# Performance work log

Measured on AMD Instinct MI355X. Metric: run time of the kernel, lower is better.

The kernel has to match this reference:

```python
import jax, jax.numpy as jnp
import numpy as np

HEAD_DIM = 64  # config['head_dim']
# dropout_prob=0.1 is a no-op in eval mode; reference computes deterministic attention.

def setup_inputs() -> dict:
    key = jax.random.key(0)
    kq, kk, kv = jax.random.split(key, 3)
    shape = (2, 12, 2048, HEAD_DIM)  # [batch, heads, seq, head_dim]
    Q = jax.random.normal(kq, shape, dtype=jnp.float32)
    K = jax.random.normal(kk, shape, dtype=jnp.float32)
    V = jax.random.normal(kv, shape, dtype=jnp.float32)
    return {"Q": Q, "K": K, "V": V}

def reference(Q, K, V):
    # dot = Q @ K^T / sqrt(head_dim); attn = softmax(dot); X = attn @ V
    scale = 1.0 / np.float32(np.sqrt(HEAD_DIM))
    dot = jnp.einsum('bhqd,bhkd->bhqk', Q, K) * scale  # [B,H,S,S]
    attn = jax.nn.softmax(dot, axis=-1)
    X = jnp.einsum('bhqk,bhkd->bhqd', attn, V)
    return X
```

## Files before the change

kernel.cpp:

```cpp
#include <hip/hip_runtime.h>
#include <hip/hip_bf16.h>

typedef __attribute__((ext_vector_type(8))) short bf16x8;
typedef __attribute__((ext_vector_type(4))) float f32x4;
typedef __attribute__((ext_vector_type(4))) unsigned short u16x4;
typedef __attribute__((ext_vector_type(2))) unsigned int u32x2;
typedef __attribute__((ext_vector_type(4))) unsigned int u32x4;
typedef __attribute__((ext_vector_type(4))) _Float16 f16x4;
typedef __attribute__((ext_vector_type(2))) __fp16 h16x2;
typedef __attribute__((ext_vector_type(4))) __fp16 h16x4;

#define SEQ 2048
#define HD 64
#define BH 24

__device__ __forceinline__ unsigned bfpack(float a, float b) {
  union { float f; unsigned u; } ua, ub; ua.f = a; ub.f = b;
  return __builtin_amdgcn_perm(ub.u + 0x8000u, ua.u + 0x8000u, 0x07060302u);
}
__device__ __forceinline__ unsigned short f2bf(float f) {
  union { float f; unsigned u; } v; v.f = f;
  unsigned r = v.u + 0x7fffu + ((v.u >> 16) & 1u);
  return (unsigned short)(r >> 16);
}

__global__ __launch_bounds__(256) void prep_kv(const float* __restrict__ K,
                                               const float* __restrict__ V,
                                               unsigned* __restrict__ Kb,
                                               _Float16* __restrict__ Vt) {
  __shared__ _Float16 t[64 * 68];
  const int bid = blockIdx.x;
  const int sb = bid >> 3;
  const int bh = (bid & 7) * 3 + (sb >> 5);
  const int k0 = (sb & 31) * 64;
  const int tid = threadIdx.x;

  const float4* ks = (const float4*)(K + ((size_t)bh * SEQ + k0) * HD);
  unsigned* kd = Kb + ((size_t)bh * SEQ + k0) * (HD / 2);
#pragma unroll
  for (int i = 0; i < 4; ++i) {
    int f = tid + i * 256;
    float4 v = ks[f];
    u32x2 o;
    o.x = bfpack(v.x, v.y);
    o.y = bfpack(v.z, v.w);
    *(u32x2*)&kd[f * 2] = o;
  }

  const float4* vs = (const float4*)(V + ((size_t)bh * SEQ + k0) * HD);
#pragma unroll
  for (int i = 0; i < 4; ++i) {
    int f = tid + i * 256;
    int k = f >> 4, cg = f & 15;
    float4 v = vs[k * 16 + cg];
    int dg = cg * 4;
    t[(dg + 0) * 68 + k] = (_Float16)v.x;
    t[(dg + 1) * 68 + k] = (_Float16)v.y;
    t[(dg + 2) * 68 + k] = (_Float16)v.z;
    t[(dg + 3) * 68 + k] = (_Float16)v.w;
  }
  __syncthreads();
  int d = tid >> 2, kg = (tid & 3) * 16;
  _Float16* g = Vt + ((size_t)(bh * 64 + d)) * SEQ + k0 + kg;
#pragma unroll
  for (int r = 0; r < 4; ++r) {
    f16x4 x = *(f16x4*)&t[d * 68 + kg + r * 4];
    *(f16x4*)&g[r * 4] = x;
  }
}

__global__ __launch_bounds__(256, 3) void attn_main(const float* __restrict__ Q,
                                                    const unsigned short* __restrict__ Kb,
                                                    const _Float16* __restrict__ Vt,
                                                    float* __restrict__ O) {
  __shared__ unsigned short kv[3][8192];

  const int tid  = threadIdx.x;
  const int lane = tid & 63;
  const int w    = tid >> 6;
  const int quad = lane >> 4;
  const int n    = lane & 15;

  const int bid = blockIdx.x;
  const int sb = bid >> 3;
  const int bh = (bid & 7) * 3 + (sb >> 5);
  const int q0 = (sb & 31) * 64;

  const float qscale = 0.125f * 1.44269504088896f;

  bf16x8 qf[4][2];
#pragma unroll
  for (int u = 0; u < 4; ++u) {
    const float* qb = Q + ((size_t)bh * SEQ + q0 + u * 16 + n) * HD;
#pragma unroll
    for (int h = 0; h < 2; ++h) {
      float4 a = *(const float4*)(qb + h * 32 + quad * 8);
      float4 b = *(const float4*)(qb + h * 32 + quad * 8 + 4);
      u32x4 pk;
      pk.x = bfpack(a.x * qscale, a.y * qscale);
      pk.y = bfpack(a.z * qscale, a.w * qscale);
      pk.z = bfpack(b.x * qscale, b.y * qscale);
      pk.w = bfpack(b.z * qscale, b.w * qscale);
      qf[u][h] = __builtin_bit_cast(bf16x8, pk);
    }
  }

  const unsigned short* Kbase = Kb + (size_t)bh * SEQ * HD;
  const unsigned short* Vbase = (const unsigned short*)(Vt + (size_t)bh * HD * SEQ);
  const unsigned short* ksrc[2];
  const unsigned short* vsrc[2];
  int soff[2];
#pragma unroll
  for (int i = 0; i < 2; ++i) {
    int s = i * 256 + tid;
    int r = s >> 3, p = s & 7, G = p ^ (r & 7);
    ksrc[i] = Kbase + r * HD + G * 8;
    vsrc[i] = Vbase + (size_t)r * SEQ + G * 8;
    soff[i] = s * 8;
  }

#define DMA_TO(buf_, it_)                                                                 \
  {                                                                                       \
    unsigned short* db_ = &kv[buf_][0];                                                   \
    _Pragma("unroll")                                                                     \
    for (int i_ = 0; i_ < 2; ++i_) {                                                      \
      __builtin_amdgcn_global_load_lds(                                                   \
          (const __attribute__((address_space(1))) void*)(ksrc[i_] + (size_t)(it_) * 4096), \
          (__attribute__((address_space(3))) void*)(db_ + soff[i_]), 16, 0, 0);           \
      __builtin_amdgcn_global_load_lds(                                                   \
          (const __attribute__((address_space(1))) void*)(vsrc[i_] + (size_t)(it_) * 64), \
          (__attribute__((address_space(3))) void*)(db_ + 4096 + soff[i_]), 16, 0, 0);    \
    }                                                                                     \
    asm volatile("" ::: "memory");                                                        \
  }

  f32x4 o[4][4];
#pragma unroll
  for (int dt = 0; dt < 4; ++dt)
#pragma unroll
    for (int u = 0; u < 4; ++u) o[dt][u] = (f32x4){0.f, 0.f, 0.f, 0.f};
  float lsum[4] = {0.f, 0.f, 0.f, 0.f};

  int ro[2];
#pragma unroll
  for (int h = 0; h < 2; ++h) ro[h] = n * 64 + (((h * 4 + quad) ^ (n & 7)) * 8);
  int vo[4];
#pragma unroll
  for (int dt = 0; dt < 4; ++dt)
    vo[dt] = dt * 1024 + n * 64 + (((w * 2 + (quad >> 1)) ^ (n & 7)) * 8) + (quad & 1) * 4;

#define COMPUTE(buf_)                                                                     \
  {                                                                                       \
    const unsigned short* kb = &kv[buf_][0];                                              \
    const unsigned short* vb = kb + 4096;                                                 \
    f32x4 s[4] = {{0,0,0,0},{0,0,0,0},{0,0,0,0},{0,0,0,0}};                               \
    _Pragma("unroll")                                                                     \
    for (int h = 0; h < 2; ++h) {                                                         \
      bf16x8 a = *(const bf16x8*)&kb[w * 1024 + ro[h]];                                   \
      _Pragma("unroll")                                                                   \
      for (int u = 0; u < 4; ++u)                                                         \
        s[u] = __builtin_amdgcn_mfma_f32_16x16x32_bf16(a, qf[u][h], s[u], 0, 0, 0);       \
    }                                                                                     \
    f16x4 pf[4];                                                                          \
    _Pragma("unroll")                                                                     \
    for (int u = 0; u < 4; ++u) {                                                         \
      float e0 = __builtin_amdgcn_exp2f(s[u][0]);                                         \
      float e1 = __builtin_amdgcn_exp2f(s[u][1]);                                         \
      float e2 = __builtin_amdgcn_exp2f(s[u][2]);                                         \
      float e3 = __builtin_amdgcn_exp2f(s[u][3]);                                         \
      lsum[u] += (e0 + e1) + (e2 + e3);                                                   \
      h16x2 a_ = __builtin_amdgcn_cvt_pkrtz(e0, e1);                                      \
      h16x2 b_ = __builtin_amdgcn_cvt_pkrtz(e2, e3);                                      \
      h16x4 ab_ = __builtin_shufflevector(a_, b_, 0, 1, 2, 3);                            \
      pf[u] = __builtin_bit_cast(f16x4, ab_);                                             \
    }                                                                                     \
    _Pragma("unroll")                                                                     \
    for (int dt = 0; dt < 4; ++dt) {                                                      \
      f16x4 vf = *(const f16x4*)((const _Float16*)vb + vo[dt]);                           \
      _Pragma("unroll")                                                                   \
      for (int u = 0; u < 4; ++u)                                                         \
        o[dt][u] = __builtin_amdgcn_mfma_f32_16x16x16f16(vf, pf[u], o[dt][u], 0, 0, 0);   \
    }                                                                                     \
  }

  DMA_TO(0, 0);
  DMA_TO(1, 1);

  int bc = 0;
  int bd = 2;
  for (int it = 0; it < 31; ++it) {
    asm volatile("s_waitcnt vmcnt(4)\n\ts_barrier" ::: "memory");
    if (it < 30) DMA_TO(bd, it + 2);
    COMPUTE(bc);
    bc = (bc == 2) ? 0 : bc + 1;
    bd = (bd == 2) ? 0 : bd + 1;
  }
  asm volatile("s_waitcnt vmcnt(0)\n\ts_barrier" ::: "memory");
  COMPUTE(bc);

#undef DMA_TO
#undef COMPUTE

#pragma unroll
  for (int u = 0; u < 4; ++u) {
    lsum[u] += __shfl_xor(lsum[u], 16);
    lsum[u] += __shfl_xor(lsum[u], 32);
  }

  float* red = (float*)&kv[0][0];
  float* lred = red + 2 * 4096;

  __syncthreads();
  if (w & 1) {
    int s = w >> 1;
#pragma unroll
    for (int dt = 0; dt < 4; ++dt)
#pragma unroll
      for (int u = 0; u < 4; ++u)
        *(f32x4*)&red[s * 4096 + (dt * 4 + u) * 256 + lane * 4] = o[dt][u];
#pragma unroll
    for (int u = 0; u < 4; ++u) lred[s * 256 + u * 64 + lane] = lsum[u];
  }
  __syncthreads();
  if (!(w & 1)) {
    int s = w >> 1;
#pragma unroll
    for (int dt = 0; dt < 4; ++dt)
#pragma unroll
      for (int u = 0; u < 4; ++u)
        o[dt][u] += *(f32x4*)&red[s * 4096 + (dt * 4 + u) * 256 + lane * 4];
#pragma unroll
    for (int u = 0; u < 4; ++u) lsum[u] += lred[s * 256 + u * 64 + lane];
  }
  __syncthreads();
  if (w == 2) {
#pragma unroll
    for (int dt = 0; dt < 4; ++dt)
#pragma unroll
      for (int u = 0; u < 4; ++u)
        *(f32x4*)&red[4096 + (dt * 4 + u) * 256 + lane * 4] = o[dt][u];
#pragma unroll
    for (int u = 0; u < 4; ++u) lred[256 + u * 64 + lane] = lsum[u];
  }
  __syncthreads();
  if (w == 0) {
#pragma unroll
    for (int dt = 0; dt < 4; ++dt)
#pragma unroll
      for (int u = 0; u < 4; ++u)
        o[dt][u] += *(f32x4*)&red[4096 + (dt * 4 + u) * 256 + lane * 4];
#pragma unroll
    for (int u = 0; u < 4; ++u) {
      float inv = 1.0f / (lsum[u] + lred[256 + u * 64 + lane]);
      float* og = O + ((size_t)bh * SEQ + q0 + u * 16 + n) * HD + quad * 4;
#pragma unroll
      for (int dt = 0; dt < 4; ++dt) {
        f32x4 r = o[dt][u];
        r.x *= inv; r.y *= inv; r.z *= inv; r.w *= inv;
        *(f32x4*)(og + dt * 16) = r;
      }
    }
  }
}

#define F_QT 128
#define F_KT 64
#define F_LD 72

__global__ __launch_bounds__(512) void attn_fwd(const float* __restrict__ Q,
                                                const float* __restrict__ K,
                                                const float* __restrict__ V,
                                                float* __restrict__ O) {
  __shared__ unsigned short sm[(F_QT + F_KT + HD + 8 * 16) * F_LD];
  unsigned short* Qs = sm;
  unsigned short* Ks = Qs + F_QT * F_LD;
  unsigned short* Vt = Ks + F_KT * F_LD;
  unsigned short* Ps = Vt + HD * F_LD;

  const int tid = threadIdx.x, lane = tid & 63, wv = tid >> 6;
  const int quad = lane >> 4, n = lane & 15;
  const int bh = blockIdx.y, q0 = blockIdx.x * F_QT;
  const float* Qg = Q + ((size_t)bh * SEQ + q0) * HD;
  const float* Kg = K + (size_t)bh * SEQ * HD;
  const float* Vg = V + (size_t)bh * SEQ * HD;
  float* Og = O + ((size_t)bh * SEQ + q0) * HD;
  const float qscale = 0.125f * 1.44269504088896f;

#pragma unroll
  for (int i = 0; i < 4; ++i) {
    int f = tid + i * 512;
    int row = f >> 4, cg = f & 15;
    float4 qv = ((const float4*)Qg)[row * 16 + cg];
    u16x4 h;
    h.x = f2bf(qv.x * qscale); h.y = f2bf(qv.y * qscale);
    h.z = f2bf(qv.z * qscale); h.w = f2bf(qv.w * qscale);
    *(u16x4*)&Qs[row * F_LD + cg * 4] = h;
  }
  __syncthreads();
  bf16x8 qf0 = *(const bf16x8*)&Qs[(wv * 16 + n) * F_LD + quad * 8];
  bf16x8 qf1 = *(const bf16x8*)&Qs[(wv * 16 + n) * F_LD + 32 + quad * 8];
  f32x4 o[4] = {{0,0,0,0},{0,0,0,0},{0,0,0,0},{0,0,0,0}};
  float mrow[4] = {-1e30f,-1e30f,-1e30f,-1e30f};
  float lrow[4] = {0.f,0.f,0.f,0.f};
  unsigned short* Pw = Ps + wv * 16 * F_LD;

  for (int it = 0; it < SEQ / F_KT; ++it) {
    __syncthreads();
    const float* Ktg = Kg + (size_t)it * F_KT * HD;
    const float* Vtg = Vg + (size_t)it * F_KT * HD;
#pragma unroll
    for (int i = 0; i < 2; ++i) {
      int f = tid + i * 512;
      int row = f >> 4, cg = f & 15;
      float4 kvv = ((const float4*)Ktg)[row * 16 + cg];
      u16x4 hk;
      hk.x = f2bf(kvv.x); hk.y = f2bf(kvv.y); hk.z = f2bf(kvv.z); hk.w = f2bf(kvv.w);
      *(u16x4*)&Ks[row * F_LD + cg * 4] = hk;
      float4 vv = ((const float4*)Vtg)[row * 16 + cg];
      Vt[(cg * 4 + 0) * F_LD + row] = f2bf(vv.x);
      Vt[(cg * 4 + 1) * F_LD + row] = f2bf(vv.y);
      Vt[(cg * 4 + 2) * F_LD + row] = f2bf(vv.z);
      Vt[(cg * 4 + 3) * F_LD + row] = f2bf(vv.w);
    }
    __syncthreads();
    f32x4 s[4];
#pragma unroll
    for (int t = 0; t < 4; ++t) {
      bf16x8 b0 = *(const bf16x8*)&Ks[(t * 16 + n) * F_LD + quad * 8];
      bf16x8 b1 = *(const bf16x8*)&Ks[(t * 16 + n) * F_LD + 32 + quad * 8];
      f32x4 c = {0,0,0,0};
      c = __builtin_amdgcn_mfma_f32_16x16x32_bf16(qf0, b0, c, 0, 0, 0);
      c = __builtin_amdgcn_mfma_f32_16x16x32_bf16(qf1, b1, c, 0, 0, 0);
      s[t] = c;
    }
    float mnew[4], alpha[4], rsum[4];
#pragma unroll
    for (int r = 0; r < 4; ++r) {
      float ml = fmaxf(fmaxf(s[0][r], s[1][r]), fmaxf(s[2][r], s[3][r]));
      ml = fmaxf(ml, __shfl_xor(ml, 1));
      ml = fmaxf(ml, __shfl_xor(ml, 2));
      ml = fmaxf(ml, __shfl_xor(ml, 4));
      ml = fmaxf(ml, __shfl_xor(ml, 8));
      mnew[r] = fmaxf(mrow[r], ml);
      alpha[r] = __builtin_amdgcn_exp2f(mrow[r] - mnew[r]);
      mrow[r] = mnew[r];
      rsum[r] = 0.f;
    }
#pragma unroll
    for (int t = 0; t < 4; ++t)
#pragma unroll
      for (int r = 0; r < 4; ++r) {
        float p = __builtin_amdgcn_exp2f(s[t][r] - mnew[r]);
        rsum[r] += p;
        Pw[(quad * 4 + r) * F_LD + t * 16 + n] = f2bf(p);
      }
#pragma unroll
    for (int r = 0; r < 4; ++r) {
      float rs = rsum[r];
      rs += __shfl_xor(rs, 1); rs += __shfl_xor(rs, 2);
      rs += __shfl_xor(rs, 4); rs += __shfl_xor(rs, 8);
      lrow[r] = lrow[r] * alpha[r] + rs;
      o[0][r] *= alpha[r]; o[1][r] *= alpha[r];
      o[2][r] *= alpha[r]; o[3][r] *= alpha[r];
    }
    asm volatile("s_waitcnt lgkmcnt(0)" ::: "memory");
    bf16x8 p0 = *(const bf16x8*)&Pw[n * F_LD + quad * 8];
    bf16x8 p1 = *(const bf16x8*)&Pw[n * F_LD + 32 + quad * 8];
#pragma unroll
    for (int t = 0; t < 4; ++t) {
      bf16x8 v0 = *(const bf16x8*)&Vt[(t * 16 + n) * F_LD + quad * 8];
      bf16x8 v1 = *(const bf16x8*)&Vt[(t * 16 + n) * F_LD + 32 + quad * 8];
      o[t] = __builtin_amdgcn_mfma_f32_16x16x32_bf16(p0, v0, o[t], 0, 0, 0);
      o[t] = __builtin_amdgcn_mfma_f32_16x16x32_bf16(p1, v1, o[t], 0, 0, 0);
    }
  }
  float inv[4];
#pragma unroll
  for (int r = 0; r < 4; ++r) inv[r] = 1.0f / lrow[r];
#pragma unroll
  for (int t = 0; t < 4; ++t)
#pragma unroll
    for (int r = 0; r < 4; ++r)
      Og[(wv * 16 + quad * 4 + r) * HD + t * 16 + n] = o[t][r] * inv[r];
}

extern "C" void kernel_launch(void* const* d_in, const int* in_sizes, int n_in,
                              void* d_out, int out_size, void* d_ws, size_t ws_size,
                              hipStream_t stream) {
  const float* Q = (const float*)d_in[0];
  const float* K = (const float*)d_in[1];
  const float* V = (const float*)d_in[2];
  float* O = (float*)d_out;

  const size_t mat = (size_t)BH * SEQ * HD;
  const size_t need = 2 * mat * sizeof(unsigned short);

  if (ws_size >= need) {
    unsigned short* Kb = (unsigned short*)d_ws;
    _Float16* Vt = (_Float16*)(Kb + mat);
    prep_kv<<<dim3(SEQ / 64 * BH), 256, 0, stream>>>(K, V, (unsigned*)Kb, Vt);
    attn_main<<<dim3(BH * SEQ / 64), 256, 0, stream>>>(Q, Kb, Vt, O);
  } else {
    attn_fwd<<<dim3(SEQ / F_QT, BH), 512, 0, stream>>>(Q, K, V, O);
  }
}
```

Measured before the change: 118.8 us.

## Give each wave a private LDS ring for its K/V slice to drop barriers

Each wave now loads only the 16 keys it consumes per iteration into its own private triple-buffered LDS region, instead of the whole block sharing one buffer. Because no wave reads another wave's data, the per-iteration s_barrier is removed and only the vmcnt wait remains. The V slice layout changes to a compact per-wave 16-key layout, so bank-conflict behaviour on V reads may differ. Waves can now drift apart, which risks uneven progress but removes the block-wide stalls.

```diff
diff --git a/kernel.cpp b/kernel.cpp
--- a/kernel.cpp
+++ b/kernel.cpp
@@ -73,7 +73,7 @@
                                                     const unsigned short* __restrict__ Kb,
                                                     const _Float16* __restrict__ Vt,
                                                     float* __restrict__ O) {
-  __shared__ unsigned short kv[3][8192];
+  __shared__ unsigned short kv[24576];
 
   const int tid  = threadIdx.x;
   const int lane = tid & 63;
@@ -105,31 +105,31 @@
     }
   }
 
+  unsigned short* kvb = &kv[w * 6144];
+
   const unsigned short* Kbase = Kb + (size_t)bh * SEQ * HD;
   const unsigned short* Vbase = (const unsigned short*)(Vt + (size_t)bh * HD * SEQ);
-  const unsigned short* ksrc[2];
-  const unsigned short* vsrc[2];
-  int soff[2];
+  const unsigned short* ksrcw[2];
+  const unsigned short* vsrcw[2];
 #pragma unroll
   for (int i = 0; i < 2; ++i) {
-    int s = i * 256 + tid;
-    int r = s >> 3, p = s & 7, G = p ^ (r & 7);
-    ksrc[i] = Kbase + r * HD + G * 8;
-    vsrc[i] = Vbase + (size_t)r * SEQ + G * 8;
-    soff[i] = s * 8;
-  }
-
-#define DMA_TO(buf_, it_)                                                                 \
+    int r = i * 8 + (lane >> 3);
+    int G = (lane & 7) ^ (r & 7);
+    ksrcw[i] = Kbase + (w * 16 + r) * HD + G * 8;
+    vsrcw[i] = Vbase + (size_t)(i * 32 + (lane >> 1)) * SEQ + w * 16 + (lane & 1) * 8;
+  }
+
+#define DMA_W(buf_, it_)                                                                  \
   {                                                                                       \
-    unsigned short* db_ = &kv[buf_][0];                                                   \
+    unsigned short* db_ = kvb + (buf_) * 2048;                                            \
     _Pragma("unroll")                                                                     \
     for (int i_ = 0; i_ < 2; ++i_) {                                                      \
       __builtin_amdgcn_global_load_lds(                                                   \
-          (const __attribute__((address_space(1))) void*)(ksrc[i_] + (size_t)(it_) * 4096), \
-          (__attribute__((address_space(3))) void*)(db_ + soff[i_]), 16, 0, 0);           \
+          (const __attribute__((address_space(1))) void*)(ksrcw[i_] + (size_t)(it_) * 4096), \
+          (__attribute__((address_space(3))) void*)(db_ + i_ * 512), 16, 0, 0);           \
       __builtin_amdgcn_global_load_lds(                                                   \
-          (const __attribute__((address_space(1))) void*)(vsrc[i_] + (size_t)(it_) * 64), \
-          (__attribute__((address_space(3))) void*)(db_ + 4096 + soff[i_]), 16, 0, 0);    \
+          (const __attribute__((address_space(1))) void*)(vsrcw[i_] + (size_t)(it_) * 64), \
+          (__attribute__((address_space(3))) void*)(db_ + 1024 + i_ * 512), 16, 0, 0);    \
     }                                                                                     \
     asm volatile("" ::: "memory");                                                        \
   }
@@ -146,17 +146,15 @@
   for (int h = 0; h < 2; ++h) ro[h] = n * 64 + (((h * 4 + quad) ^ (n & 7)) * 8);
   int vo[4];
 #pragma unroll
-  for (int dt = 0; dt < 4; ++dt)
-    vo[dt] = dt * 1024 + n * 64 + (((w * 2 + (quad >> 1)) ^ (n & 7)) * 8) + (quad & 1) * 4;
-
-#define COMPUTE(buf_)                                                                     \
+  for (int dt = 0; dt < 4; ++dt) vo[dt] = 1024 + (dt * 16 + n) * 16 + quad * 4;
+
+#define COMPUTE_W(buf_)                                                                   \
   {                                                                                       \
-    const unsigned short* kb = &kv[buf_][0];                                              \
-    const unsigned short* vb = kb + 4096;                                                 \
+    const unsigned short* kb = kvb + (buf_) * 2048;                                       \
     f32x4 s[4] = {{0,0,0,0},{0,0,0,0},{0,0,0,0},{0,0,0,0}};                               \
     _Pragma("unroll")                                                                     \
     for (int h = 0; h < 2; ++h) {                                                         \
-      bf16x8 a = *(const bf16x8*)&kb[w * 1024 + ro[h]];                                   \
+      bf16x8 a = *(const bf16x8*)&kb[ro[h]];                                              \
       _Pragma("unroll")                                                                   \
       for (int u = 0; u < 4; ++u)                                                         \
         s[u] = __builtin_amdgcn_mfma_f32_16x16x32_bf16(a, qf[u][h], s[u], 0, 0, 0);       \
@@ -176,30 +174,30 @@
     }                                                                                     \
     _Pragma("unroll")                                                                     \
     for (int dt = 0; dt < 4; ++dt) {                                                      \
-      f16x4 vf = *(const f16x4*)((const _Float16*)vb + vo[dt]);                           \
+      f16x4 vf = *(const f16x4*)((const _Float16*)kb + vo[dt]);                           \
       _Pragma("unroll")                                                                   \
       for (int u = 0; u < 4; ++u)                                                         \
         o[dt][u] = __builtin_amdgcn_mfma_f32_16x16x16f16(vf, pf[u], o[dt][u], 0, 0, 0);   \
     }                                                                                     \
   }
 
-  DMA_TO(0, 0);
-  DMA_TO(1, 1);
+  DMA_W(0, 0);
+  DMA_W(1, 1);
 
   int bc = 0;
   int bd = 2;
   for (int it = 0; it < 31; ++it) {
-    asm volatile("s_waitcnt vmcnt(4)\n\ts_barrier" ::: "memory");
-    if (it < 30) DMA_TO(bd, it + 2);
-    COMPUTE(bc);
+    asm volatile("s_waitcnt vmcnt(4)" ::: "memory");
+    if (it < 30) DMA_W(bd, it + 2);
+    COMPUTE_W(bc);
     bc = (bc == 2) ? 0 : bc + 1;
     bd = (bd == 2) ? 0 : bd + 1;
   }
-  asm volatile("s_waitcnt vmcnt(0)\n\ts_barrier" ::: "memory");
-  COMPUTE(bc);
-
-#undef DMA_TO
-#undef COMPUTE
+  asm volatile("s_waitcnt vmcnt(0)" ::: "memory");
+  COMPUTE_W(bc);
+
+#undef DMA_W
+#undef COMPUTE_W
 
 #pragma unroll
   for (int u = 0; u < 4; ++u) {
@@ -207,7 +205,7 @@
     lsum[u] += __shfl_xor(lsum[u], 32);
   }
 
-  float* red = (float*)&kv[0][0];
+  float* red = (float*)&kv[0];
   float* lred = red + 2 * 4096;
 
   __syncthreads();
```

New measurement: 122.4 us. +3.0%, slower.

## Pair KV tiles to use 16x16x32 f16 MFMA for the PV product

Applied to the files above, without the earlier changes.

The main loop now processes KV tiles in pairs. The first tile's softmax probabilities and V fragments are held in registers, and the second tile's are concatenated with them into 8-wide operands, so PV uses the 16x16x32 f16 MFMA instead of two 16x16x16 calls. This halves the number of PV MFMA instructions and changes loop structure and register liveness. In exchange it raises register pressure, adds an explicit lgkmcnt wait, and extends the live range of the V data across a barrier.

```diff
diff --git a/kernel.cpp b/kernel.cpp
--- a/kernel.cpp
+++ b/kernel.cpp
@@ -7,6 +7,7 @@
 typedef __attribute__((ext_vector_type(2))) unsigned int u32x2;
 typedef __attribute__((ext_vector_type(4))) unsigned int u32x4;
 typedef __attribute__((ext_vector_type(4))) _Float16 f16x4;
+typedef __attribute__((ext_vector_type(8))) _Float16 f16x8;
 typedef __attribute__((ext_vector_type(2))) __fp16 h16x2;
 typedef __attribute__((ext_vector_type(4))) __fp16 h16x4;
 
@@ -149,10 +150,12 @@
   for (int dt = 0; dt < 4; ++dt)
     vo[dt] = dt * 1024 + n * 64 + (((w * 2 + (quad >> 1)) ^ (n & 7)) * 8) + (quad & 1) * 4;
 
-#define COMPUTE(buf_)                                                                     \
+  f16x4 pA[4];
+  f16x4 vA[4];
+
+#define QK_SM(buf_, pf_)                                                                  \
   {                                                                                       \
     const unsigned short* kb = &kv[buf_][0];                                              \
-    const unsigned short* vb = kb + 4096;                                                 \
     f32x4 s[4] = {{0,0,0,0},{0,0,0,0},{0,0,0,0},{0,0,0,0}};                               \
     _Pragma("unroll")                                                                     \
     for (int h = 0; h < 2; ++h) {                                                         \
@@ -161,7 +164,6 @@
       for (int u = 0; u < 4; ++u)                                                         \
         s[u] = __builtin_amdgcn_mfma_f32_16x16x32_bf16(a, qf[u][h], s[u], 0, 0, 0);       \
     }                                                                                     \
-    f16x4 pf[4];                                                                          \
     _Pragma("unroll")                                                                     \
     for (int u = 0; u < 4; ++u) {                                                         \
       float e0 = __builtin_amdgcn_exp2f(s[u][0]);                                         \
@@ -172,14 +174,35 @@
       h16x2 a_ = __builtin_amdgcn_cvt_pkrtz(e0, e1);                                      \
       h16x2 b_ = __builtin_amdgcn_cvt_pkrtz(e2, e3);                                      \
       h16x4 ab_ = __builtin_shufflevector(a_, b_, 0, 1, 2, 3);                            \
-      pf[u] = __builtin_bit_cast(f16x4, ab_);                                             \
+      pf_[u] = __builtin_bit_cast(f16x4, ab_);                                            \
     }                                                                                     \
+  }
+
+#define COMPUTE_EVEN(buf_)                                                                \
+  {                                                                                       \
+    QK_SM(buf_, pA);                                                                      \
+    const _Float16* vb_ = (const _Float16*)(&kv[buf_][0] + 4096);                         \
+    _Pragma("unroll")                                                                     \
+    for (int dt = 0; dt < 4; ++dt) vA[dt] = *(const f16x4*)(vb_ + vo[dt]);                \
+    asm volatile("s_waitcnt lgkmcnt(0)" ::: "memory");                                    \
+  }
+
+#define COMPUTE_ODD(buf_)                                                                 \
+  {                                                                                       \
+    f16x4 pB[4];                                                                          \
+    QK_SM(buf_, pB);                                                                      \
+    const _Float16* vb_ = (const _Float16*)(&kv[buf_][0] + 4096);                         \
+    f16x8 bp[4];                                                                          \
+    _Pragma("unroll")                                                                     \
+    for (int u = 0; u < 4; ++u)                                                           \
+      bp[u] = __builtin_shufflevector(pA[u], pB[u], 0, 1, 2, 3, 4, 5, 6, 7);              \
     _Pragma("unroll")                                                                     \
     for (int dt = 0; dt < 4; ++dt) {                                                      \
-      f16x4 vf = *(const f16x4*)((const _Float16*)vb + vo[dt]);                           \
+      f16x4 vB = *(const f16x4*)(vb_ + vo[dt]);                                           \
+      f16x8 av = __builtin_shufflevector(vA[dt], vB, 0, 1, 2, 3, 4, 5, 6, 7);             \
       _Pragma("unroll")                                                                   \
       for (int u = 0; u < 4; ++u)                                                         \
-        o[dt][u] = __builtin_amdgcn_mfma_f32_16x16x16f16(vf, pf[u], o[dt][u], 0, 0, 0);   \
+        o[dt][u] = __builtin_amdgcn_mfma_f32_16x16x32_f16(av, bp[u], o[dt][u], 0, 0, 0);  \
     }                                                                                     \
   }
 
@@ -188,18 +211,28 @@
 
   int bc = 0;
   int bd = 2;
-  for (int it = 0; it < 31; ++it) {
+  for (int t = 0; t < 15; ++t) {
     asm volatile("s_waitcnt vmcnt(4)\n\ts_barrier" ::: "memory");
-    if (it < 30) DMA_TO(bd, it + 2);
-    COMPUTE(bc);
+    DMA_TO(bd, 2 * t + 2);
+    COMPUTE_EVEN(bc);
     bc = (bc == 2) ? 0 : bc + 1;
     bd = (bd == 2) ? 0 : bd + 1;
-  }
+    asm volatile("s_waitcnt vmcnt(4)\n\ts_barrier" ::: "memory");
+    DMA_TO(bd, 2 * t + 3);
+    COMPUTE_ODD(bc);
+    bc = (bc == 2) ? 0 : bc + 1;
+    bd = (bd == 2) ? 0 : bd + 1;
+  }
+  asm volatile("s_waitcnt vmcnt(4)\n\ts_barrier" ::: "memory");
+  COMPUTE_EVEN(bc);
+  bc = (bc == 2) ? 0 : bc + 1;
   asm volatile("s_waitcnt vmcnt(0)\n\ts_barrier" ::: "memory");
-  COMPUTE(bc);
+  COMPUTE_ODD(bc);
 
 #undef DMA_TO
-#undef COMPUTE
+#undef QK_SM
+#undef COMPUTE_EVEN
+#undef COMPUTE_ODD
 
 #pragma unroll
   for (int u = 0; u < 4; ++u) {
```

Measured after the change: 122.1 us. 2.8% more time.
